# Performance work log

Hardware: AMD Instinct MI355X
Metric: run time of the kernel (lower is better)

## Reference

```python
import jax, jax.numpy as jnp
import numpy as np
from jax import lax

B = 512
MBD_B, MBD_C = 64, 16
FEAT = 40 * 4 * 4  # 640


def _conv(x, w, b):
    y = lax.conv_general_dilated(x, w, (1, 1), 'VALID',
                                 dimension_numbers=('NCHW', 'OIHW', 'NCHW'))
    return y + b[None, :, None, None]


def _maxpool2(x):
    return lax.reduce_window(x, -jnp.inf, lax.max,
                             (1, 1, 2, 2), (1, 1, 2, 2), 'VALID')


def setup_inputs() -> dict:
    key = jax.random.key(0)
    ks = jax.random.split(key, 10)
    def he(k, shape, fan_in):
        return jax.random.normal(k, shape, dtype=jnp.float32) * np.float32(1.0 / np.sqrt(fan_in))
    return {
        'x': jax.random.normal(ks[0], (B, 1, 28, 28), dtype=jnp.float32),
        'conv1_w': he(ks[1], (20, 1, 5, 5), 25),
        'conv1_b': jnp.zeros((20,), jnp.float32),
        'conv2_w': he(ks[2], (40, 20, 5, 5), 20 * 25),
        'conv2_b': jnp.zeros((40,), jnp.float32),
        'T': he(ks[3], (MBD_B * MBD_C, FEAT), FEAT),          # feature_scan_tensor (no bias)
        'fc1_w': he(ks[4], (100, FEAT + MBD_B), FEAT + MBD_B),
        'fc1_b': jnp.zeros((100,), jnp.float32),
        'fc2_w': he(ks[5], (1, 100), 100),
        'fc2_b': jnp.zeros((1,), jnp.float32),
    }


def reference(x, conv1_w, conv1_b, conv2_w, conv2_b, T, fc1_w, fc1_b, fc2_w, fc2_b):
    # conv feature extractor: [B,1,28,28] -> [B,40,4,4]
    h = _maxpool2(jax.nn.relu(_conv(x, conv1_w, conv1_b)))
    h = _maxpool2(jax.nn.relu(_conv(h, conv2_w, conv2_b)))
    feats = h.reshape(h.shape[0], -1)  # [B, 640]

    # minibatch discrimination: M = feats @ T^T -> [B, b, c]
    M = (feats @ T.T).reshape(-1, MBD_B, MBD_C)
    # pairwise L1 over c: [B, B, b] (includes j==i diagonal = 0, exp(0)=1, as in original)
    dist = jnp.abs(M[:, None, :, :] - M[None, :, :, :]).sum(axis=3)
    closeness = jnp.exp(-dist).sum(axis=1)  # [B, b]

    out = jnp.concatenate([feats, closeness], axis=1)  # [B, 640+b]
    out = jax.nn.relu(out @ fc1_w.T + fc1_b)
    # Dropout(p=0.2) omitted (deterministic eval-mode reference)
    out = jax.nn.sigmoid(out @ fc2_w.T + fc2_b)  # [B, 1]
    return out
```

## Files before the change

kernel.cpp:

```cpp
#include <hip/hip_runtime.h>


typedef __attribute__((ext_vector_type(8))) short bf16x8;
typedef __attribute__((ext_vector_type(4))) float f32x4;

static __device__ __forceinline__ unsigned short f2bf(float x) {
  unsigned int u = __float_as_uint(x);
  unsigned int r = (u + 0x7fffu + ((u >> 16) & 1u)) >> 16;
  return (unsigned short)r;
}
static __device__ __forceinline__ float bf2f(unsigned short h) {
  return __uint_as_float(((unsigned int)h) << 16);
}

__global__ __launch_bounds__(256) void kP_prep(
    const float* __restrict__ c2w, const float* __restrict__ T,
    float* __restrict__ ws2, unsigned short* __restrict__ Th,
    unsigned short* __restrict__ Tl) {
  const int idx = blockIdx.x * 256 + threadIdx.x;
  if (idx < 655360) {
    const float v = T[idx];
    const unsigned short h = f2bf(v);
    Th[idx] = h;
    Tl[idx] = f2bf(v - bf2f(h));
  }
  if (idx < 32000) {
    const int ic = idx / 1600;
    const int r = idx - ic * 1600;
    const int tap = r >> 6;
    const int slot = r & 63;
    const int grp = slot >> 3;
    const int q = slot & 7;
    float val = 0.f;
    if (q < 5) val = c2w[(grp * 5 + q) * 500 + ic * 25 + tap];
    ws2[idx] = val;
  }
}

__global__ __launch_bounds__(256) void kC_conv(
    const float* __restrict__ x, const float* __restrict__ c1w,
    const float* __restrict__ c1b, const float* __restrict__ ws2,
    const float* __restrict__ c2b, float* __restrict__ feats,
    unsigned short* __restrict__ fh, unsigned short* __restrict__ fl) {
  __shared__ __align__(16) float img[784];
  __shared__ __align__(16) float h1s[2880];
  __shared__ float wl1[500];
  __shared__ float bl1[20];
  __shared__ float bl2[40];
  __shared__ __align__(16) float wl2[2][2][1600];
  __shared__ float mg[128][21];

  const int tid = threadIdx.x;
  const int imgId = blockIdx.x;

  {
    float4* dst = reinterpret_cast<float4*>(img);
    const float4* src = reinterpret_cast<const float4*>(x + imgId * 784);
    for (int t = tid; t < 196; t += 256) dst[t] = src[t];
  }
  for (int t = tid; t < 500; t += 256) wl1[t] = c1w[t];
  if (tid < 20) bl1[tid] = c1b[tid];
  if (tid >= 64 && tid < 104) bl2[tid - 64] = c2b[tid - 64];
  __syncthreads();

  for (int qd = tid; qd < 720; qd += 256) {
    const int ch = qd / 36;
    const int rem = qd - ch * 36;
    const int py = rem / 3;
    const int qx = rem - py * 3;
    const int r0 = py * 2;
    const int c0 = qx * 8;
    float p[6][12];
#pragma unroll
    for (int r = 0; r < 6; ++r) {
      const float* ib = &img[(r0 + r) * 28 + c0];
      const float4 a = *reinterpret_cast<const float4*>(ib);
      const float4 b = *reinterpret_cast<const float4*>(ib + 4);
      const float4 c = *reinterpret_cast<const float4*>(ib + 8);
      p[r][0] = a.x; p[r][1] = a.y; p[r][2] = a.z; p[r][3] = a.w;
      p[r][4] = b.x; p[r][5] = b.y; p[r][6] = b.z; p[r][7] = b.w;
      p[r][8] = c.x; p[r][9] = c.y; p[r][10] = c.z; p[r][11] = c.w;
    }
    float s[16];
#pragma unroll
    for (int u = 0; u < 16; ++u) s[u] = 0.f;
    const float* wc = &wl1[ch * 25];
#pragma unroll
    for (int ky = 0; ky < 5; ++ky) {
#pragma unroll
      for (int kx = 0; kx < 5; ++kx) {
        const float w = wc[ky * 5 + kx];
#pragma unroll
        for (int u = 0; u < 4; ++u) {
#pragma unroll
          for (int dy = 0; dy < 2; ++dy) {
#pragma unroll
            for (int dx = 0; dx < 2; ++dx) {
              s[u * 4 + dy * 2 + dx] += p[ky + dy][2 * u + dx + kx] * w;
            }
          }
        }
      }
    }
    const float bb = bl1[ch];
    float4 o;
    o.x = fmaxf(fmaxf(fmaxf(s[0], s[1]), fmaxf(s[2], s[3])) + bb, 0.f);
    o.y = fmaxf(fmaxf(fmaxf(s[4], s[5]), fmaxf(s[6], s[7])) + bb, 0.f);
    o.z = fmaxf(fmaxf(fmaxf(s[8], s[9]), fmaxf(s[10], s[11])) + bb, 0.f);
    o.w = fmaxf(fmaxf(fmaxf(s[12], s[13]), fmaxf(s[14], s[15])) + bb, 0.f);
    *reinterpret_cast<float4*>(&h1s[ch * 144 + py * 12 + qx * 4]) = o;
  }

  float4* wlf4 = reinterpret_cast<float4*>(&wl2[0][0][0]);
  const float4* wsf4 = reinterpret_cast<const float4*>(ws2);
#pragma unroll
  for (int k = 0; k < 4; ++k) {
    const int e = tid + k * 256;
    if (e < 800) {
      const int str = e / 400;
      const int i4 = e - str * 400;
      wlf4[(str * 2 + 0) * 400 + i4] = wsf4[(str * 10 + 0) * 400 + i4];
    }
  }
  __syncthreads();

  const int h = tid >> 7;
  const int grp = (tid >> 4) & 7;
  const int pos = tid & 15;
  const int oy = (pos >> 2) * 2;
  const int ox = (pos & 3) * 2;
  float acc[5][4];
#pragma unroll
  for (int q = 0; q < 5; ++q)
#pragma unroll
    for (int u = 0; u < 4; ++u) acc[q][u] = 0.f;

  for (int s = 0; s < 10; ++s) {
    const int p0 = s & 1;
    float4 sv[4];
    if (s < 9) {
#pragma unroll
      for (int k = 0; k < 4; ++k) {
        const int e = tid + k * 256;
        if (e < 800) {
          const int str = e / 400;
          const int i4 = e - str * 400;
          sv[k] = wsf4[(str * 10 + s + 1) * 400 + i4];
        }
      }
    }
    const int ic = h * 10 + s;
    float p[6][6];
    {
      const float* ib = &h1s[ic * 144 + oy * 12 + ox];
#pragma unroll
      for (int r = 0; r < 6; ++r) {
        const float2 v0 = *reinterpret_cast<const float2*>(&ib[r * 12 + 0]);
        const float2 v1 = *reinterpret_cast<const float2*>(&ib[r * 12 + 2]);
        const float2 v2 = *reinterpret_cast<const float2*>(&ib[r * 12 + 4]);
        p[r][0] = v0.x; p[r][1] = v0.y; p[r][2] = v1.x;
        p[r][3] = v1.y; p[r][4] = v2.x; p[r][5] = v2.y;
      }
    }
    const float* wbase = &wl2[h][p0][0];
#pragma unroll
    for (int ky = 0; ky < 5; ++ky) {
#pragma unroll
      for (int kx = 0; kx < 5; ++kx) {
        const int tap = ky * 5 + kx;
        const float4 w4 =
            *reinterpret_cast<const float4*>(&wbase[tap * 64 + grp * 8]);
        const float w4b = wbase[tap * 64 + grp * 8 + 4];
        const float i00 = p[ky][kx];
        const float i01 = p[ky][kx + 1];
        const float i10 = p[ky + 1][kx];
        const float i11 = p[ky + 1][kx + 1];
        acc[0][0] += i00 * w4.x; acc[0][1] += i01 * w4.x;
        acc[0][2] += i10 * w4.x; acc[0][3] += i11 * w4.x;
        acc[1][0] += i00 * w4.y; acc[1][1] += i01 * w4.y;
        acc[1][2] += i10 * w4.y; acc[1][3] += i11 * w4.y;
        acc[2][0] += i00 * w4.z; acc[2][1] += i01 * w4.z;
        acc[2][2] += i10 * w4.z; acc[2][3] += i11 * w4.z;
        acc[3][0] += i00 * w4.w; acc[3][1] += i01 * w4.w;
        acc[3][2] += i10 * w4.w; acc[3][3] += i11 * w4.w;
        acc[4][0] += i00 * w4b; acc[4][1] += i01 * w4b;
        acc[4][2] += i10 * w4b; acc[4][3] += i11 * w4b;
      }
    }
    if (s < 9) {
#pragma unroll
      for (int k = 0; k < 4; ++k) {
        const int e = tid + k * 256;
        if (e < 800) {
          const int str = e / 400;
          const int i4 = e - str * 400;
          wlf4[(str * 2 + ((s + 1) & 1)) * 400 + i4] = sv[k];
        }
      }
    }
    __syncthreads();
  }

  const int midx = grp * 16 + pos;
  if (h == 1) {
#pragma unroll
    for (int q = 0; q < 5; ++q)
#pragma unroll
      for (int u = 0; u < 4; ++u) mg[midx][q * 4 + u] = acc[q][u];
  }
  __syncthreads();
  if (h == 0) {
#pragma unroll
    for (int q = 0; q < 5; ++q) {
      const int ch = grp * 5 + q;
      const float a0 = acc[q][0] + mg[midx][q * 4 + 0];
      const float a1 = acc[q][1] + mg[midx][q * 4 + 1];
      const float a2 = acc[q][2] + mg[midx][q * 4 + 2];
      const float a3 = acc[q][3] + mg[midx][q * 4 + 3];
      const float r0v =
          fmaxf(fmaxf(fmaxf(a0, a1), fmaxf(a2, a3)) + bl2[ch], 0.f);
      const int off = imgId * 640 + ch * 16 + pos;
      feats[off] = r0v;
      const unsigned short h0 = f2bf(r0v);
      fh[off] = h0;
      fl[off] = f2bf(r0v - bf2f(h0));
    }
  }
}

__global__ __launch_bounds__(256) void k3m_gemm(
    const unsigned short* __restrict__ fh, const unsigned short* __restrict__ fl,
    const unsigned short* __restrict__ Th, const unsigned short* __restrict__ Tl,
    float* __restrict__ M) {
  const int tid = threadIdx.x;
  const int w = tid >> 6;
  const int l = tid & 63;
  const int fr = l & 15;
  const int hi = l >> 4;
  const int if0 = blockIdx.x >> 4;
  const int jf = (blockIdx.x & 15) * 4 + w;
  const int abase = (if0 * 16 + fr) * 640 + hi * 8;
  const int bbase = (jf * 16 + fr) * 640 + hi * 8;

  f32x4 acc = (f32x4){0.f, 0.f, 0.f, 0.f};
#pragma unroll
  for (int kk = 0; kk < 20; ++kk) {
    const int ko = kk * 32;
    const bf16x8 aH = *reinterpret_cast<const bf16x8*>(fh + abase + ko);
    const bf16x8 aL = *reinterpret_cast<const bf16x8*>(fl + abase + ko);
    const bf16x8 bH = *reinterpret_cast<const bf16x8*>(Th + bbase + ko);
    const bf16x8 bL = *reinterpret_cast<const bf16x8*>(Tl + bbase + ko);
    acc = __builtin_amdgcn_mfma_f32_16x16x32_bf16(aH, bH, acc, 0, 0, 0);
    acc = __builtin_amdgcn_mfma_f32_16x16x32_bf16(aL, bH, acc, 0, 0, 0);
    acc = __builtin_amdgcn_mfma_f32_16x16x32_bf16(aH, bL, acc, 0, 0, 0);
  }
#pragma unroll
  for (int r = 0; r < 4; ++r) {
    M[(if0 * 16 + hi * 4 + r) * 1024 + jf * 16 + fr] = acc[r];
  }
}

__global__ __launch_bounds__(256) void k4_mbd(const float* __restrict__ M,
                                              float* __restrict__ cp) {
  __shared__ float4 jb4[2][4][256];
  const int bid = blockIdx.x;
  const int ig = bid >> 4;
  const int jq = bid & 15;
  const int t = threadIdx.x;
  const int b = t & 63;
  const int g = t >> 6;
  const int i0 = ig * 16 + g * 4;
  const float4* Mf4 = reinterpret_cast<const float4*>(M);

  float4 mi[4][4];
#pragma unroll
  for (int u = 0; u < 4; ++u) {
#pragma unroll
    for (int q = 0; q < 4; ++q) mi[u][q] = Mf4[(i0 + u) * 256 + b * 4 + q];
  }
  const int wslot = (t >> 2) * 4 + ((t & 3) ^ ((t >> 3) & 3));
  {
#pragma unroll
    for (int k = 0; k < 4; ++k)
      jb4[0][k][wslot] = Mf4[(jq * 32 + k) * 256 + t];
  }
  __syncthreads();

  float acc[4] = {0.f, 0.f, 0.f, 0.f};
  const int xr = (b >> 1) & 3;
  for (int c = 0; c < 8; ++c) {
    float4 st[4];
    if (c < 7) {
#pragma unroll
      for (int k = 0; k < 4; ++k)
        st[k] = Mf4[(jq * 32 + (c + 1) * 4 + k) * 256 + t];
    }
    const int cbuf = c & 1;
#pragma unroll
    for (int jj = 0; jj < 4; ++jj) {
      const float4* rowp = jb4[cbuf][jj];
      float4 mj[4];
#pragma unroll
      for (int q = 0; q < 4; ++q) mj[q] = rowp[b * 4 + (q ^ xr)];
#pragma unroll
      for (int u = 0; u < 4; ++u) {
        float dist =
            fabsf(mi[u][0].x - mj[0].x) + fabsf(mi[u][0].y - mj[0].y) +
            fabsf(mi[u][0].z - mj[0].z) + fabsf(mi[u][0].w - mj[0].w) +
            fabsf(mi[u][1].x - mj[1].x) + fabsf(mi[u][1].y - mj[1].y) +
            fabsf(mi[u][1].z - mj[1].z) + fabsf(mi[u][1].w - mj[1].w) +
            fabsf(mi[u][2].x - mj[2].x) + fabsf(mi[u][2].y - mj[2].y) +
            fabsf(mi[u][2].z - mj[2].z) + fabsf(mi[u][2].w - mj[2].w) +
            fabsf(mi[u][3].x - mj[3].x) + fabsf(mi[u][3].y - mj[3].y) +
            fabsf(mi[u][3].z - mj[3].z) + fabsf(mi[u][3].w - mj[3].w);
        acc[u] += __expf(-dist);
      }
    }
    if (c < 7) {
#pragma unroll
      for (int k = 0; k < 4; ++k) jb4[(c + 1) & 1][k][wslot] = st[k];
    }
    __syncthreads();
  }
#pragma unroll
  for (int u = 0; u < 4; ++u)
    cp[(jq * 512 + i0 + u) * 64 + b] = acc[u];
}

__global__ __launch_bounds__(256) void k5_head(
    const float* __restrict__ feats, const float* __restrict__ cp,
    const float* __restrict__ w1, const float* __restrict__ b1,
    const float* __restrict__ w2, const float* __restrict__ b2,
    float* __restrict__ out) {
  __shared__ __align__(16) float v[704];
  __shared__ float hb[100];
  const int i = blockIdx.x;
  const int tid = threadIdx.x;
  float4* v4 = reinterpret_cast<float4*>(v);
  if (tid < 160)
    v4[tid] = reinterpret_cast<const float4*>(feats + i * 640)[tid];
  if (tid >= 192) {
    const int bb = tid - 192;
    float s = 0.f;
#pragma unroll
    for (int q = 0; q < 16; ++q) s += cp[(q * 512 + i) * 64 + bb];
    v[640 + bb] = s;
  }
  __syncthreads();
  const int wave = tid >> 6;
  const int lane = tid & 63;
  for (int r = wave; r < 100; r += 4) {
    const float4* wr = reinterpret_cast<const float4*>(w1 + r * 704);
    const float4 wa = wr[lane];
    const float4 wb = wr[lane + 64];
    const float4 va = v4[lane];
    const float4 vb = v4[lane + 64];
    float s = wa.x * va.x + wa.y * va.y + wa.z * va.z + wa.w * va.w +
              wb.x * vb.x + wb.y * vb.y + wb.z * vb.z + wb.w * vb.w;
    if (lane < 48) {
      const float4 wc = wr[lane + 128];
      const float4 vc = v4[lane + 128];
      s += wc.x * vc.x + wc.y * vc.y + wc.z * vc.z + wc.w * vc.w;
    }
#pragma unroll
    for (int off = 32; off; off >>= 1) s += __shfl_xor(s, off);
    if (lane == 0) hb[r] = fmaxf(s + b1[r], 0.f) * w2[r];
  }
  __syncthreads();
  if (tid < 64) {
    float s = hb[tid] + ((tid < 36) ? hb[tid + 64] : 0.f);
#pragma unroll
    for (int off = 32; off; off >>= 1) s += __shfl_xor(s, off);
    if (tid == 0) out[i] = 1.f / (1.f + __expf(-(s + b2[0])));
  }
}

extern "C" void kernel_launch(void* const* d_in, const int* in_sizes, int n_in,
                              void* d_out, int out_size, void* d_ws,
                              size_t ws_size, hipStream_t stream) {
  const float* x   = (const float*)d_in[0];
  const float* c1w = (const float*)d_in[1];
  const float* c1b = (const float*)d_in[2];
  const float* c2w = (const float*)d_in[3];
  const float* c2b = (const float*)d_in[4];
  const float* T   = (const float*)d_in[5];
  const float* f1w = (const float*)d_in[6];
  const float* f1b = (const float*)d_in[7];
  const float* f2w = (const float*)d_in[8];
  const float* f2b = (const float*)d_in[9];
  float* out = (float*)d_out;

  float* feats = (float*)d_ws;
  float* M     = feats + 327680;
  float* cp    = M + 524288;
  float* ws2   = cp + 524288;
  unsigned short* fh = (unsigned short*)(ws2 + 32000);
  unsigned short* fl = fh + 327680;
  unsigned short* Th = fl + 327680;
  unsigned short* Tl = Th + 655360;

  kP_prep<<<2560, 256, 0, stream>>>(c2w, T, ws2, Th, Tl);
  kC_conv<<<512, 256, 0, stream>>>(x, c1w, c1b, ws2, c2b, feats, fh, fl);
  k3m_gemm<<<512, 256, 0, stream>>>(fh, fl, Th, Tl, M);
  k4_mbd<<<512, 256, 0, stream>>>(M, cp);
  k5_head<<<512, 256, 0, stream>>>(feats, cp, f1w, f1b, f2w, f2b, out);
}
```

Measured before the change: 178.0 us.

## Restructure conv kernel to read wave-uniform weights from global and drop LDS weight staging

The conv kernel no longer stages conv1/conv2 weights in shared memory with double buffering and per-step barriers. Instead each wave owns a fixed channel group (5 conv1 channels, 10 conv2 channels) and reads wave-uniform weights directly from repacked global buffers prepared in the prep kernel. Conv2 now computes one pre-pool output per lane over all 20 input channels and pools with cross-lane shuffles, which removes the cross-half LDS reduction and most __syncthreads. This cuts LDS footprint and synchronization, but relies on scalar/cached global loads for weights and changes the per-thread work split.

```diff
diff --git a/kernel.cpp b/kernel.cpp
--- a/kernel.cpp
+++ b/kernel.cpp
@@ -14,8 +14,9 @@
 }
 
 __global__ __launch_bounds__(256) void kP_prep(
-    const float* __restrict__ c2w, const float* __restrict__ T,
-    float* __restrict__ ws2, unsigned short* __restrict__ Th,
+    const float* __restrict__ c1w, const float* __restrict__ c2w,
+    const float* __restrict__ T, float* __restrict__ ws2,
+    float* __restrict__ c1ws, unsigned short* __restrict__ Th,
     unsigned short* __restrict__ Tl) {
   const int idx = blockIdx.x * 256 + threadIdx.x;
   if (idx < 655360) {
@@ -24,201 +25,160 @@
     Th[idx] = h;
     Tl[idx] = f2bf(v - bf2f(h));
   }
-  if (idx < 32000) {
-    const int ic = idx / 1600;
-    const int r = idx - ic * 1600;
-    const int tap = r >> 6;
-    const int slot = r & 63;
-    const int grp = slot >> 3;
-    const int q = slot & 7;
+  if (idx < 24000) {
+    const int w = idx / 6000;
+    const int r = idx - w * 6000;
+    const int ic = r / 300;
+    const int r2 = r - ic * 300;
+    const int tap = r2 / 12;
+    const int sl = r2 - tap * 12;
     float val = 0.f;
-    if (q < 5) val = c2w[(grp * 5 + q) * 500 + ic * 25 + tap];
+    if (sl < 10) val = c2w[(w * 10 + sl) * 500 + ic * 25 + tap];
     ws2[idx] = val;
   }
+  if (idx < 800) {
+    const int w = idx / 200;
+    const int r = idx - w * 200;
+    const int tap = r >> 3;
+    const int c = r & 7;
+    float val = 0.f;
+    if (c < 5) val = c1w[(w * 5 + c) * 25 + tap];
+    c1ws[idx] = val;
+  }
 }
 
 __global__ __launch_bounds__(256) void kC_conv(
-    const float* __restrict__ x, const float* __restrict__ c1w,
+    const float* __restrict__ x, const float* __restrict__ c1ws,
     const float* __restrict__ c1b, const float* __restrict__ ws2,
     const float* __restrict__ c2b, float* __restrict__ feats,
     unsigned short* __restrict__ fh, unsigned short* __restrict__ fl) {
   __shared__ __align__(16) float img[784];
   __shared__ __align__(16) float h1s[2880];
-  __shared__ float wl1[500];
-  __shared__ float bl1[20];
-  __shared__ float bl2[40];
-  __shared__ __align__(16) float wl2[2][2][1600];
-  __shared__ float mg[128][21];
 
   const int tid = threadIdx.x;
   const int imgId = blockIdx.x;
+  const int wid = __builtin_amdgcn_readfirstlane(tid >> 6);
+  const int l = tid & 63;
 
   {
     float4* dst = reinterpret_cast<float4*>(img);
     const float4* src = reinterpret_cast<const float4*>(x + imgId * 784);
     for (int t = tid; t < 196; t += 256) dst[t] = src[t];
   }
-  for (int t = tid; t < 500; t += 256) wl1[t] = c1w[t];
-  if (tid < 20) bl1[tid] = c1b[tid];
-  if (tid >= 64 && tid < 104) bl2[tid - 64] = c2b[tid - 64];
-  __syncthreads();
-
-  for (int qd = tid; qd < 720; qd += 256) {
-    const int ch = qd / 36;
-    const int rem = qd - ch * 36;
-    const int py = rem / 3;
-    const int qx = rem - py * 3;
-    const int r0 = py * 2;
-    const int c0 = qx * 8;
-    float p[6][12];
-#pragma unroll
-    for (int r = 0; r < 6; ++r) {
-      const float* ib = &img[(r0 + r) * 28 + c0];
-      const float4 a = *reinterpret_cast<const float4*>(ib);
-      const float4 b = *reinterpret_cast<const float4*>(ib + 4);
-      const float4 c = *reinterpret_cast<const float4*>(ib + 8);
-      p[r][0] = a.x; p[r][1] = a.y; p[r][2] = a.z; p[r][3] = a.w;
-      p[r][4] = b.x; p[r][5] = b.y; p[r][6] = b.z; p[r][7] = b.w;
-      p[r][8] = c.x; p[r][9] = c.y; p[r][10] = c.z; p[r][11] = c.w;
-    }
-    float s[16];
-#pragma unroll
-    for (int u = 0; u < 16; ++u) s[u] = 0.f;
-    const float* wc = &wl1[ch * 25];
-#pragma unroll
-    for (int ky = 0; ky < 5; ++ky) {
-#pragma unroll
-      for (int kx = 0; kx < 5; ++kx) {
-        const float w = wc[ky * 5 + kx];
-#pragma unroll
-        for (int u = 0; u < 4; ++u) {
-#pragma unroll
-          for (int dy = 0; dy < 2; ++dy) {
-#pragma unroll
-            for (int dx = 0; dx < 2; ++dx) {
-              s[u * 4 + dy * 2 + dx] += p[ky + dy][2 * u + dx + kx] * w;
-            }
-          }
+  __syncthreads();
+
+  const float* __restrict__ w1b = c1ws + wid * 200;
+#pragma unroll 1
+  for (int pi = 0; pi < 3; ++pi) {
+    const int posidx = pi * 64 + l;
+    if (posidx < 144) {
+      const int py = posidx / 12;
+      const int px = posidx - py * 12;
+      float pv[6][6];
+      const float* ib = &img[py * 2 * 28 + px * 2];
+#pragma unroll
+      for (int r = 0; r < 6; ++r) {
+        const float2 a = *reinterpret_cast<const float2*>(&ib[r * 28 + 0]);
+        const float2 b = *reinterpret_cast<const float2*>(&ib[r * 28 + 2]);
+        const float2 c = *reinterpret_cast<const float2*>(&ib[r * 28 + 4]);
+        pv[r][0] = a.x; pv[r][1] = a.y; pv[r][2] = b.x;
+        pv[r][3] = b.y; pv[r][4] = c.x; pv[r][5] = c.y;
+      }
+      float acc[5][4];
+#pragma unroll
+      for (int c = 0; c < 5; ++c)
+#pragma unroll
+        for (int u = 0; u < 4; ++u) acc[c][u] = 0.f;
+#pragma unroll
+      for (int ky = 0; ky < 5; ++ky) {
+#pragma unroll
+        for (int kx = 0; kx < 5; ++kx) {
+          const int tap = ky * 5 + kx;
+          const float4 wv = *reinterpret_cast<const float4*>(&w1b[tap * 8]);
+          const float w4 = w1b[tap * 8 + 4];
+          const float i00 = pv[ky][kx];
+          const float i01 = pv[ky][kx + 1];
+          const float i10 = pv[ky + 1][kx];
+          const float i11 = pv[ky + 1][kx + 1];
+          acc[0][0] += i00 * wv.x; acc[0][1] += i01 * wv.x;
+          acc[0][2] += i10 * wv.x; acc[0][3] += i11 * wv.x;
+          acc[1][0] += i00 * wv.y; acc[1][1] += i01 * wv.y;
+          acc[1][2] += i10 * wv.y; acc[1][3] += i11 * wv.y;
+          acc[2][0] += i00 * wv.z; acc[2][1] += i01 * wv.z;
+          acc[2][2] += i10 * wv.z; acc[2][3] += i11 * wv.z;
+          acc[3][0] += i00 * wv.w; acc[3][1] += i01 * wv.w;
+          acc[3][2] += i10 * wv.w; acc[3][3] += i11 * wv.w;
+          acc[4][0] += i00 * w4; acc[4][1] += i01 * w4;
+          acc[4][2] += i10 * w4; acc[4][3] += i11 * w4;
         }
       }
-    }
-    const float bb = bl1[ch];
-    float4 o;
-    o.x = fmaxf(fmaxf(fmaxf(s[0], s[1]), fmaxf(s[2], s[3])) + bb, 0.f);
-    o.y = fmaxf(fmaxf(fmaxf(s[4], s[5]), fmaxf(s[6], s[7])) + bb, 0.f);
-    o.z = fmaxf(fmaxf(fmaxf(s[8], s[9]), fmaxf(s[10], s[11])) + bb, 0.f);
-    o.w = fmaxf(fmaxf(fmaxf(s[12], s[13]), fmaxf(s[14], s[15])) + bb, 0.f);
-    *reinterpret_cast<float4*>(&h1s[ch * 144 + py * 12 + qx * 4]) = o;
-  }
-
-  float4* wlf4 = reinterpret_cast<float4*>(&wl2[0][0][0]);
-  const float4* wsf4 = reinterpret_cast<const float4*>(ws2);
-#pragma unroll
-  for (int k = 0; k < 4; ++k) {
-    const int e = tid + k * 256;
-    if (e < 800) {
-      const int str = e / 400;
-      const int i4 = e - str * 400;
-      wlf4[(str * 2 + 0) * 400 + i4] = wsf4[(str * 10 + 0) * 400 + i4];
-    }
-  }
-  __syncthreads();
-
-  const int h = tid >> 7;
-  const int grp = (tid >> 4) & 7;
-  const int pos = tid & 15;
-  const int oy = (pos >> 2) * 2;
-  const int ox = (pos & 3) * 2;
-  float acc[5][4];
-#pragma unroll
-  for (int q = 0; q < 5; ++q)
-#pragma unroll
-    for (int u = 0; u < 4; ++u) acc[q][u] = 0.f;
-
-  for (int s = 0; s < 10; ++s) {
-    const int p0 = s & 1;
-    float4 sv[4];
-    if (s < 9) {
-#pragma unroll
-      for (int k = 0; k < 4; ++k) {
-        const int e = tid + k * 256;
-        if (e < 800) {
-          const int str = e / 400;
-          const int i4 = e - str * 400;
-          sv[k] = wsf4[(str * 10 + s + 1) * 400 + i4];
-        }
-      }
-    }
-    const int ic = h * 10 + s;
-    float p[6][6];
+#pragma unroll
+      for (int c = 0; c < 5; ++c) {
+        const float m =
+            fmaxf(fmaxf(acc[c][0], acc[c][1]), fmaxf(acc[c][2], acc[c][3])) +
+            c1b[wid * 5 + c];
+        h1s[(wid * 5 + c) * 144 + posidx] = fmaxf(m, 0.f);
+      }
+    }
+  }
+  __syncthreads();
+
+  const int cy = l >> 3;
+  const int cx = l & 7;
+  const int s = cx & ~1;
+  const bool dsh = (cx & 1) != 0;
+  float acc[10];
+#pragma unroll
+  for (int q = 0; q < 10; ++q) acc[q] = 0.f;
+
+  const float* __restrict__ w2b = ws2 + wid * 6000;
+#pragma unroll 1
+  for (int ic = 0; ic < 20; ++ic) {
+    float pd[5][5];
     {
-      const float* ib = &h1s[ic * 144 + oy * 12 + ox];
-#pragma unroll
-      for (int r = 0; r < 6; ++r) {
-        const float2 v0 = *reinterpret_cast<const float2*>(&ib[r * 12 + 0]);
-        const float2 v1 = *reinterpret_cast<const float2*>(&ib[r * 12 + 2]);
-        const float2 v2 = *reinterpret_cast<const float2*>(&ib[r * 12 + 4]);
-        p[r][0] = v0.x; p[r][1] = v0.y; p[r][2] = v1.x;
-        p[r][3] = v1.y; p[r][4] = v2.x; p[r][5] = v2.y;
-      }
-    }
-    const float* wbase = &wl2[h][p0][0];
+      const float* ib = &h1s[ic * 144 + cy * 12 + s];
+#pragma unroll
+      for (int r = 0; r < 5; ++r) {
+        const float2 a = *reinterpret_cast<const float2*>(&ib[r * 12 + 0]);
+        const float2 b = *reinterpret_cast<const float2*>(&ib[r * 12 + 2]);
+        const float2 c = *reinterpret_cast<const float2*>(&ib[r * 12 + 4]);
+        pd[r][0] = dsh ? a.y : a.x;
+        pd[r][1] = dsh ? b.x : a.y;
+        pd[r][2] = dsh ? b.y : b.x;
+        pd[r][3] = dsh ? c.x : b.y;
+        pd[r][4] = dsh ? c.y : c.x;
+      }
+    }
+    const float* wt = w2b + ic * 300;
 #pragma unroll
     for (int ky = 0; ky < 5; ++ky) {
 #pragma unroll
       for (int kx = 0; kx < 5; ++kx) {
         const int tap = ky * 5 + kx;
-        const float4 w4 =
-            *reinterpret_cast<const float4*>(&wbase[tap * 64 + grp * 8]);
-        const float w4b = wbase[tap * 64 + grp * 8 + 4];
-        const float i00 = p[ky][kx];
-        const float i01 = p[ky][kx + 1];
-        const float i10 = p[ky + 1][kx];
-        const float i11 = p[ky + 1][kx + 1];
-        acc[0][0] += i00 * w4.x; acc[0][1] += i01 * w4.x;
-        acc[0][2] += i10 * w4.x; acc[0][3] += i11 * w4.x;
-        acc[1][0] += i00 * w4.y; acc[1][1] += i01 * w4.y;
-        acc[1][2] += i10 * w4.y; acc[1][3] += i11 * w4.y;
-        acc[2][0] += i00 * w4.z; acc[2][1] += i01 * w4.z;
-        acc[2][2] += i10 * w4.z; acc[2][3] += i11 * w4.z;
-        acc[3][0] += i00 * w4.w; acc[3][1] += i01 * w4.w;
-        acc[3][2] += i10 * w4.w; acc[3][3] += i11 * w4.w;
-        acc[4][0] += i00 * w4b; acc[4][1] += i01 * w4b;
-        acc[4][2] += i10 * w4b; acc[4][3] += i11 * w4b;
-      }
-    }
-    if (s < 9) {
-#pragma unroll
-      for (int k = 0; k < 4; ++k) {
-        const int e = tid + k * 256;
-        if (e < 800) {
-          const int str = e / 400;
-          const int i4 = e - str * 400;
-          wlf4[(str * 2 + ((s + 1) & 1)) * 400 + i4] = sv[k];
-        }
-      }
-    }
-    __syncthreads();
-  }
-
-  const int midx = grp * 16 + pos;
-  if (h == 1) {
-#pragma unroll
-    for (int q = 0; q < 5; ++q)
-#pragma unroll
-      for (int u = 0; u < 4; ++u) mg[midx][q * 4 + u] = acc[q][u];
-  }
-  __syncthreads();
-  if (h == 0) {
-#pragma unroll
-    for (int q = 0; q < 5; ++q) {
-      const int ch = grp * 5 + q;
-      const float a0 = acc[q][0] + mg[midx][q * 4 + 0];
-      const float a1 = acc[q][1] + mg[midx][q * 4 + 1];
-      const float a2 = acc[q][2] + mg[midx][q * 4 + 2];
-      const float a3 = acc[q][3] + mg[midx][q * 4 + 3];
-      const float r0v =
-          fmaxf(fmaxf(fmaxf(a0, a1), fmaxf(a2, a3)) + bl2[ch], 0.f);
+        const float4 w03 = *reinterpret_cast<const float4*>(&wt[tap * 12]);
+        const float4 w47 = *reinterpret_cast<const float4*>(&wt[tap * 12 + 4]);
+        const float2 w89 = *reinterpret_cast<const float2*>(&wt[tap * 12 + 8]);
+        const float iv = pd[ky][kx];
+        acc[0] += iv * w03.x; acc[1] += iv * w03.y;
+        acc[2] += iv * w03.z; acc[3] += iv * w03.w;
+        acc[4] += iv * w47.x; acc[5] += iv * w47.y;
+        acc[6] += iv * w47.z; acc[7] += iv * w47.w;
+        acc[8] += iv * w89.x; acc[9] += iv * w89.y;
+      }
+    }
+  }
+
+#pragma unroll
+  for (int q = 0; q < 10; ++q) {
+    acc[q] = fmaxf(acc[q], __shfl_xor(acc[q], 1));
+    acc[q] = fmaxf(acc[q], __shfl_xor(acc[q], 8));
+  }
+  if ((l & 9) == 0) {
+    const int pos = (cy >> 1) * 4 + (cx >> 1);
+#pragma unroll
+    for (int q = 0; q < 10; ++q) {
+      const int ch = wid * 10 + q;
+      const float r0v = fmaxf(acc[q] + c2b[ch], 0.f);
       const int off = imgId * 640 + ch * 16 + pos;
       feats[off] = r0v;
       const unsigned short h0 = f2bf(r0v);
@@ -394,13 +354,14 @@
   float* M     = feats + 327680;
   float* cp    = M + 524288;
   float* ws2   = cp + 524288;
-  unsigned short* fh = (unsigned short*)(ws2 + 32000);
+  float* c1ws  = ws2 + 24000;
+  unsigned short* fh = (unsigned short*)(c1ws + 800);
   unsigned short* fl = fh + 327680;
   unsigned short* Th = fl + 327680;
   unsigned short* Tl = Th + 655360;
 
-  kP_prep<<<2560, 256, 0, stream>>>(c2w, T, ws2, Th, Tl);
-  kC_conv<<<512, 256, 0, stream>>>(x, c1w, c1b, ws2, c2b, feats, fh, fl);
+  kP_prep<<<2560, 256, 0, stream>>>(c1w, c2w, T, ws2, c1ws, Th, Tl);
+  kC_conv<<<512, 256, 0, stream>>>(x, c1ws, c1b, ws2, c2b, feats, fh, fl);
   k3m_gemm<<<512, 256, 0, stream>>>(fh, fl, Th, Tl, M);
   k4_mbd<<<512, 256, 0, stream>>>(M, cp);
   k5_head<<<512, 256, 0, stream>>>(feats, cp, f1w, f1b, f2w, f2b, out);
```

Measured after the change: 195.9 us. +10.1%, slower.

## Rewrite FC head as split-bf16 MFMA GEMM and halve rows per MBD block

Applied to the files above, without the earlier changes.

The fc1 head changes from a per-sample dot-product kernel with 512 blocks into a tiled GEMM over 64 samples per block. It uses bf16 hi/lo MFMA with a three-term split, and fc1 weights are converted to bf16 hi/lo in the prep kernel. The MBD kernel now processes 2 rows per thread instead of 4 and launches 1024 blocks, trading per-thread reuse for more parallelism. With only 8 blocks the head runs on very few CUs, and the bf16x3 split slightly changes numerics.

```diff
diff --git a/kernel.cpp b/kernel.cpp
--- a/kernel.cpp
+++ b/kernel.cpp
@@ -15,14 +15,23 @@
 
 __global__ __launch_bounds__(256) void kP_prep(
     const float* __restrict__ c2w, const float* __restrict__ T,
-    float* __restrict__ ws2, unsigned short* __restrict__ Th,
-    unsigned short* __restrict__ Tl) {
+    const float* __restrict__ w1, float* __restrict__ ws2,
+    unsigned short* __restrict__ Th, unsigned short* __restrict__ Tl,
+    unsigned short* __restrict__ w1h, unsigned short* __restrict__ w1l) {
   const int idx = blockIdx.x * 256 + threadIdx.x;
   if (idx < 655360) {
     const float v = T[idx];
     const unsigned short h = f2bf(v);
     Th[idx] = h;
     Tl[idx] = f2bf(v - bf2f(h));
+  }
+  if (idx < 78848) {
+    const int row = idx / 704;
+    const int col = idx - row * 704;
+    const float v = (row < 100) ? w1[row * 704 + col] : 0.f;
+    const unsigned short h = f2bf(v);
+    w1h[idx] = h;
+    w1l[idx] = f2bf(v - bf2f(h));
   }
   if (idx < 32000) {
     const int ic = idx / 1600;
@@ -269,12 +278,12 @@
   const int t = threadIdx.x;
   const int b = t & 63;
   const int g = t >> 6;
-  const int i0 = ig * 16 + g * 4;
+  const int i0 = ig * 8 + g * 2;
   const float4* Mf4 = reinterpret_cast<const float4*>(M);
 
-  float4 mi[4][4];
-#pragma unroll
-  for (int u = 0; u < 4; ++u) {
+  float4 mi[2][4];
+#pragma unroll
+  for (int u = 0; u < 2; ++u) {
 #pragma unroll
     for (int q = 0; q < 4; ++q) mi[u][q] = Mf4[(i0 + u) * 256 + b * 4 + q];
   }
@@ -286,7 +295,7 @@
   }
   __syncthreads();
 
-  float acc[4] = {0.f, 0.f, 0.f, 0.f};
+  float acc[2] = {0.f, 0.f};
   const int xr = (b >> 1) & 3;
   for (int c = 0; c < 8; ++c) {
     float4 st[4];
@@ -303,7 +312,7 @@
 #pragma unroll
       for (int q = 0; q < 4; ++q) mj[q] = rowp[b * 4 + (q ^ xr)];
 #pragma unroll
-      for (int u = 0; u < 4; ++u) {
+      for (int u = 0; u < 2; ++u) {
         float dist =
             fabsf(mi[u][0].x - mj[0].x) + fabsf(mi[u][0].y - mj[0].y) +
             fabsf(mi[u][0].z - mj[0].z) + fabsf(mi[u][0].w - mj[0].w) +
@@ -323,55 +332,102 @@
     __syncthreads();
   }
 #pragma unroll
-  for (int u = 0; u < 4; ++u)
+  for (int u = 0; u < 2; ++u)
     cp[(jq * 512 + i0 + u) * 64 + b] = acc[u];
 }
 
 __global__ __launch_bounds__(256) void k5_head(
-    const float* __restrict__ feats, const float* __restrict__ cp,
-    const float* __restrict__ w1, const float* __restrict__ b1,
+    const unsigned short* __restrict__ fh, const unsigned short* __restrict__ fl,
+    const float* __restrict__ cp, const unsigned short* __restrict__ w1h,
+    const unsigned short* __restrict__ w1l, const float* __restrict__ b1,
     const float* __restrict__ w2, const float* __restrict__ b2,
     float* __restrict__ out) {
-  __shared__ __align__(16) float v[704];
-  __shared__ float hb[100];
-  const int i = blockIdx.x;
+  __shared__ __align__(16) unsigned short clh[64][72];
+  __shared__ __align__(16) unsigned short cll[64][72];
+  const int i0 = blockIdx.x * 64;
   const int tid = threadIdx.x;
-  float4* v4 = reinterpret_cast<float4*>(v);
-  if (tid < 160)
-    v4[tid] = reinterpret_cast<const float4*>(feats + i * 640)[tid];
-  if (tid >= 192) {
-    const int bb = tid - 192;
+
+#pragma unroll 1
+  for (int k = 0; k < 16; ++k) {
+    const int e = tid + k * 256;
+    const int im = e >> 6, bb = e & 63;
     float s = 0.f;
 #pragma unroll
-    for (int q = 0; q < 16; ++q) s += cp[(q * 512 + i) * 64 + bb];
-    v[640 + bb] = s;
+    for (int jq = 0; jq < 16; ++jq) s += cp[(jq * 512 + i0 + im) * 64 + bb];
+    const unsigned short h0 = f2bf(s);
+    clh[im][bb] = h0;
+    cll[im][bb] = f2bf(s - bf2f(h0));
   }
   __syncthreads();
-  const int wave = tid >> 6;
-  const int lane = tid & 63;
-  for (int r = wave; r < 100; r += 4) {
-    const float4* wr = reinterpret_cast<const float4*>(w1 + r * 704);
-    const float4 wa = wr[lane];
-    const float4 wb = wr[lane + 64];
-    const float4 va = v4[lane];
-    const float4 vb = v4[lane + 64];
-    float s = wa.x * va.x + wa.y * va.y + wa.z * va.z + wa.w * va.w +
-              wb.x * vb.x + wb.y * vb.y + wb.z * vb.z + wb.w * vb.w;
-    if (lane < 48) {
-      const float4 wc = wr[lane + 128];
-      const float4 vc = v4[lane + 128];
-      s += wc.x * vc.x + wc.y * vc.y + wc.z * vc.z + wc.w * vc.w;
-    }
-#pragma unroll
-    for (int off = 32; off; off >>= 1) s += __shfl_xor(s, off);
-    if (lane == 0) hb[r] = fmaxf(s + b1[r], 0.f) * w2[r];
-  }
-  __syncthreads();
-  if (tid < 64) {
-    float s = hb[tid] + ((tid < 36) ? hb[tid + 64] : 0.f);
-#pragma unroll
-    for (int off = 32; off; off >>= 1) s += __shfl_xor(s, off);
-    if (tid == 0) out[i] = 1.f / (1.f + __expf(-(s + b2[0])));
+
+  const int w = tid >> 6;
+  const int l = tid & 63;
+  const int fr = l & 15;
+  const int hi = l >> 4;
+  const int im0 = w * 16;
+  const int arow = (i0 + im0 + fr) * 640 + hi * 8;
+
+  f32x4 acc[7];
+#pragma unroll
+  for (int js = 0; js < 7; ++js) acc[js] = (f32x4){0.f, 0.f, 0.f, 0.f};
+
+#pragma unroll 1
+  for (int ks = 0; ks < 20; ++ks) {
+    const int ko = ks * 32;
+    const bf16x8 aH = *reinterpret_cast<const bf16x8*>(fh + arow + ko);
+    const bf16x8 aL = *reinterpret_cast<const bf16x8*>(fl + arow + ko);
+#pragma unroll
+    for (int js = 0; js < 7; ++js) {
+      const int brow = (js * 16 + fr) * 704 + ko + hi * 8;
+      const bf16x8 bH = *reinterpret_cast<const bf16x8*>(w1h + brow);
+      const bf16x8 bL = *reinterpret_cast<const bf16x8*>(w1l + brow);
+      acc[js] = __builtin_amdgcn_mfma_f32_16x16x32_bf16(aH, bH, acc[js], 0, 0, 0);
+      acc[js] = __builtin_amdgcn_mfma_f32_16x16x32_bf16(aL, bH, acc[js], 0, 0, 0);
+      acc[js] = __builtin_amdgcn_mfma_f32_16x16x32_bf16(aH, bL, acc[js], 0, 0, 0);
+    }
+  }
+#pragma unroll
+  for (int ks = 0; ks < 2; ++ks) {
+    const int co = ks * 32 + hi * 8;
+    const bf16x8 aH = *reinterpret_cast<const bf16x8*>(&clh[im0 + fr][co]);
+    const bf16x8 aL = *reinterpret_cast<const bf16x8*>(&cll[im0 + fr][co]);
+#pragma unroll
+    for (int js = 0; js < 7; ++js) {
+      const int brow = (js * 16 + fr) * 704 + 640 + co;
+      const bf16x8 bH = *reinterpret_cast<const bf16x8*>(w1h + brow);
+      const bf16x8 bL = *reinterpret_cast<const bf16x8*>(w1l + brow);
+      acc[js] = __builtin_amdgcn_mfma_f32_16x16x32_bf16(aH, bH, acc[js], 0, 0, 0);
+      acc[js] = __builtin_amdgcn_mfma_f32_16x16x32_bf16(aL, bH, acc[js], 0, 0, 0);
+      acc[js] = __builtin_amdgcn_mfma_f32_16x16x32_bf16(aH, bL, acc[js], 0, 0, 0);
+    }
+  }
+
+  float s4[4] = {0.f, 0.f, 0.f, 0.f};
+#pragma unroll
+  for (int js = 0; js < 7; ++js) {
+    const int col = js * 16 + fr;
+    if (col < 100) {
+      const float bb = b1[col];
+      const float ww = w2[col];
+#pragma unroll
+      for (int reg = 0; reg < 4; ++reg) {
+        const float v = fmaxf(acc[js][reg] + bb, 0.f);
+        s4[reg] += v * ww;
+      }
+    }
+  }
+#pragma unroll
+  for (int off = 1; off <= 8; off <<= 1) {
+#pragma unroll
+    for (int reg = 0; reg < 4; ++reg) s4[reg] += __shfl_xor(s4[reg], off);
+  }
+  if (fr == 0) {
+    const float bb2 = b2[0];
+#pragma unroll
+    for (int reg = 0; reg < 4; ++reg) {
+      out[i0 + im0 + hi * 4 + reg] =
+          1.f / (1.f + __expf(-(s4[reg] + bb2)));
+    }
   }
 }
 
@@ -394,14 +450,16 @@
   float* M     = feats + 327680;
   float* cp    = M + 524288;
   float* ws2   = cp + 524288;
-  unsigned short* fh = (unsigned short*)(ws2 + 32000);
-  unsigned short* fl = fh + 327680;
-  unsigned short* Th = fl + 327680;
-  unsigned short* Tl = Th + 655360;
-
-  kP_prep<<<2560, 256, 0, stream>>>(c2w, T, ws2, Th, Tl);
+  unsigned short* fh  = (unsigned short*)(ws2 + 32000);
+  unsigned short* fl  = fh + 327680;
+  unsigned short* Th  = fl + 327680;
+  unsigned short* Tl  = Th + 655360;
+  unsigned short* w1h = Tl + 655360;
+  unsigned short* w1l = w1h + 78848;
+
+  kP_prep<<<2560, 256, 0, stream>>>(c2w, T, f1w, ws2, Th, Tl, w1h, w1l);
   kC_conv<<<512, 256, 0, stream>>>(x, c1w, c1b, ws2, c2b, feats, fh, fl);
   k3m_gemm<<<512, 256, 0, stream>>>(fh, fl, Th, Tl, M);
-  k4_mbd<<<512, 256, 0, stream>>>(M, cp);
-  k5_head<<<512, 256, 0, stream>>>(feats, cp, f1w, f1b, f2w, f2b, out);
-}
+  k4_mbd<<<1024, 256, 0, stream>>>(M, cp);
+  k5_head<<<8, 256, 0, stream>>>(fh, fl, cp, w1h, w1l, f1b, f2w, f2b, out);
+}
```

Measured after the change: 208.2 us. 1.17x slower.
